# Performance work log

Measured on AMD Instinct MI355X. Metric: run time of the kernel, lower is better.

## Reference

```python
import jax, jax.numpy as jnp
import numpy as np

N_NODES = 100000
N_EDGES = 1600000
N_GRAPHS = 256
IN_C = 64
HID = 128
OUT = 128
BN_EPS = 1e-5


def setup_inputs() -> dict:
    key = jax.random.key(0)
    ks = jax.random.split(key, 24)
    x = jax.random.normal(ks[0], (N_NODES, IN_C), jnp.float32)
    edge_index = jax.random.randint(ks[1], (2, N_EDGES), 0, N_NODES, dtype=jnp.int64 if jax.config.jax_enable_x64 else jnp.int32)
    batch = jnp.sort(jax.random.randint(ks[2], (N_NODES,), 0, N_GRAPHS))

    def lin(k, i, o):
        return (jax.random.normal(k, (i, o), jnp.float32) / np.float32(np.sqrt(i)))

    d = {"x": x, "edge_index": edge_index, "batch": batch}
    in_dims = [IN_C, HID, HID]
    for l in range(3):
        d[f"w1_{l}"] = lin(ks[3 + 6 * l], in_dims[l], HID)
        d[f"b1_{l}"] = jnp.zeros((HID,), jnp.float32)
        d[f"w2_{l}"] = lin(ks[4 + 6 * l], HID, HID)
        d[f"b2_{l}"] = jnp.zeros((HID,), jnp.float32)
        d[f"gamma_{l}"] = jnp.ones((HID,), jnp.float32)
        d[f"beta_{l}"] = jnp.zeros((HID,), jnp.float32)
    d["proj_w"] = lin(ks[22], HID, OUT)
    d["proj_b"] = jnp.zeros((OUT,), jnp.float32)
    return d


def _gin_forward(x, edge_index, batch, layers, proj_w, proj_b):
    src, dst = edge_index[0], edge_index[1]
    h = x
    for (w1, b1, w2, b2, g, b) in layers:
        # GINConv (eps=0, aggr='add'): MLP(h_i + sum_{j->i} h_j)
        agg = jax.ops.segment_sum(h[src], dst, num_segments=h.shape[0])
        z = h + agg
        z = jax.nn.relu(z @ w1 + b1) @ w2 + b2
        # BatchNorm1d, training mode (biased batch stats)
        mean = z.mean(axis=0)
        var = z.var(axis=0)
        z = (z - mean) * jax.lax.rsqrt(var + BN_EPS) * g + b
        h = jax.nn.relu(z)
    # global_mean_pool over graph ids
    s = jax.ops.segment_sum(h, batch, num_segments=N_GRAPHS)
    cnt = jax.ops.segment_sum(jnp.ones((h.shape[0], 1), h.dtype), batch, num_segments=N_GRAPHS)
    hg = s / jnp.maximum(cnt, 1.0)
    return hg @ proj_w + proj_b


def reference(x, edge_index, batch,
              w1_0, b1_0, w2_0, b2_0, gamma_0, beta_0,
              w1_1, b1_1, w2_1, b2_1, gamma_1, beta_1,
              w1_2, b1_2, w2_2, b2_2, gamma_2, beta_2,
              proj_w, proj_b):
    layers = [
        (w1_0, b1_0, w2_0, b2_0, gamma_0, beta_0),
        (w1_1, b1_1, w2_1, b2_1, gamma_1, beta_1),
        (w1_2, b1_2, w2_2, b2_2, gamma_2, beta_2),
    ]
    return _gin_forward(x, edge_index, batch, layers, proj_w, proj_b)
```

## Files before the change

kernel.cpp:

```cpp
#include <hip/hip_runtime.h>

#define N_NODES 100000
#define N_EDGES 1600000
#define N_GRAPHS 256
#define HID 128
#define BN_EPS 1e-5f

#define NT 1563
#define EB 4096
#define RB 391
#define PB 1563

typedef __bf16 bf16x8 __attribute__((ext_vector_type(8)));
typedef __bf16 bf16x4 __attribute__((ext_vector_type(4)));
typedef __bf16 bf16x2 __attribute__((ext_vector_type(2)));
typedef float f32x4 __attribute__((ext_vector_type(4)));

__global__ __launch_bounds__(256) void setup_kernel(
    const float* __restrict__ x, __bf16* __restrict__ xb,
    const float* __restrict__ wa, const float* __restrict__ wb,
    const float* __restrict__ wc, const float* __restrict__ wd,
    const float* __restrict__ we, const float* __restrict__ wf,
    __bf16* __restrict__ wt,
    const int* __restrict__ batch, int* __restrict__ counts,
    const int* __restrict__ ei, int* __restrict__ tcnt) {
  __shared__ int hist[NT];
  int b = blockIdx.x;
  if (b < 6250) {
    int idx = b * 256 + threadIdx.x;
    if (idx >= N_NODES * 16) return;
    f32x4 v = ((const f32x4*)x)[idx];
    bf16x4 o = {(__bf16)v[0], (__bf16)v[1], (__bf16)v[2], (__bf16)v[3]};
    ((bf16x4*)xb)[idx] = o;
  } else if (b < 6250 + 352) {
    int idx = (b - 6250) * 256 + threadIdx.x;
    if (idx >= 90112) return;
    const float* w;
    int K, local;
    if (idx < 8192) { w = wa; K = 64; local = idx; }
    else {
      int s = (idx - 8192) / 16384;
      local = (idx - 8192) - s * 16384;
      K = 128;
      w = (s == 0) ? wb : (s == 1) ? wc : (s == 2) ? wd : (s == 3) ? we : wf;
    }
    int n = local / K, k = local - n * K;
    wt[idx] = (__bf16)w[k * 128 + n];
  } else if (b < 6609) {
    int t = (b - 6602) * 256 + threadIdx.x;
    int r0 = t * 64;
    if (r0 >= N_NODES) return;
    int rend = min(r0 + 64, N_NODES);
    int curg = batch[r0], cnt = 0;
    for (int r = r0; r < rend; r++) {
      int g = batch[r];
      if (g != curg) {
        atomicAdd(&counts[curg], cnt);
        curg = g;
        cnt = 1;
      } else {
        cnt++;
      }
    }
    atomicAdd(&counts[curg], cnt);
  } else {
    int t = threadIdx.x;
    for (int i = t; i < NT; i += 256) hist[i] = 0;
    __syncthreads();
    int base = (b - 6609) * EB;
#pragma unroll 4
    for (int i = 0; i < EB / 256; i++) {
      int e = base + i * 256 + t;
      if (e < N_EDGES) atomicAdd(&hist[ei[N_EDGES + e] >> 6], 1);
    }
    __syncthreads();
    for (int i = t; i < NT; i += 256) {
      int h = hist[i];
      if (h) atomicAdd(&tcnt[i], h);
    }
  }
}

__global__ __launch_bounds__(256) void tile_scan_kernel(const int* __restrict__ tcnt,
                                                        int* __restrict__ tstart,
                                                        int* __restrict__ gcursor) {
  __shared__ int ps[256];
  int t = threadIdx.x;
  const int CH = (NT + 255) / 256;
  int lo = t * CH, hi = min(lo + CH, NT);
  int s = 0;
  for (int i = lo; i < hi; i++) s += tcnt[i];
  ps[t] = s;
  __syncthreads();
  for (int off = 1; off < 256; off <<= 1) {
    int v = ps[t];
    int u = (t >= off) ? ps[t - off] : 0;
    __syncthreads();
    ps[t] = v + u;
    __syncthreads();
  }
  int base = (t == 0) ? 0 : ps[t - 1];
  for (int i = lo; i < hi; i++) {
    tstart[i] = base;
    gcursor[i] = base;
    base += tcnt[i];
  }
  if (t == 0) tstart[NT] = N_EDGES;
}

__global__ __launch_bounds__(256) void reorder2_kernel(const int* __restrict__ ei,
                                                       int* __restrict__ gcursor,
                                                       int* __restrict__ epack) {
  __shared__ int hist[NT];
  int t = threadIdx.x;
  for (int i = t; i < NT; i += 256) hist[i] = 0;
  __syncthreads();
  int base = blockIdx.x * EB;
#pragma unroll 4
  for (int i = 0; i < EB / 256; i++) {
    int e = base + i * 256 + t;
    if (e < N_EDGES) atomicAdd(&hist[ei[N_EDGES + e] >> 6], 1);
  }
  __syncthreads();
  for (int i = t; i < NT; i += 256) {
    int h = hist[i];
    if (h) hist[i] = atomicAdd(&gcursor[i], h);
  }
  __syncthreads();
#pragma unroll 4
  for (int i = 0; i < EB / 256; i++) {
    int e = base + i * 256 + t;
    if (e < N_EDGES) {
      int d = ei[N_EDGES + e];
      int s = ei[e];
      int pos = atomicAdd(&hist[d >> 6], 1);
      epack[pos] = (s << 6) | (d & 63);
    }
  }
}

__global__ __launch_bounds__(256) void row_sort_kernel(const int* __restrict__ tstart,
                                                       const int* __restrict__ epack,
                                                       int* __restrict__ starts,
                                                       int* __restrict__ srcs) {
  __shared__ int cnt[64];
  __shared__ int rbase[65];
  __shared__ int rofs[64];
  int t = threadIdx.x, b = blockIdx.x;
  int ts = tstart[b], te = tstart[b + 1];
  if (t < 64) cnt[t] = 0;
  __syncthreads();
  for (int i = ts + t; i < te; i += 256) atomicAdd(&cnt[epack[i] & 63], 1);
  __syncthreads();
  if (t == 0) {
    int a = 0;
    for (int r = 0; r < 64; r++) { rbase[r] = a; a += cnt[r]; }
    rbase[64] = a;
  }
  __syncthreads();
  if (t < 64) rofs[t] = ts + rbase[t];
  if (t <= 64) {
    int gr = b * 64 + t;
    if (gr <= N_NODES) starts[gr] = ts + rbase[t];
  }
  __syncthreads();
  for (int i = ts + t; i < te; i += 256) {
    int p = epack[i];
    int pos = atomicAdd(&rofs[p & 63], 1);
    srcs[pos] = p >> 6;
  }
}

template <int C, bool BN>
__global__ __launch_bounds__(256) void gather_kernel(const __bf16* __restrict__ h,
                                                     const float* __restrict__ accum,
                                                     const float* __restrict__ gamma,
                                                     const float* __restrict__ beta,
                                                     const int* __restrict__ starts,
                                                     const int* __restrict__ srcs,
                                                     __bf16* __restrict__ z) {
  const int lane = threadIdx.x & 63;
  const int row = __builtin_amdgcn_readfirstlane(blockIdx.x * 4 + (threadIdx.x >> 6));
  const int e0 = starts[row], e1 = starts[row + 1];

  if constexpr (C == 128) {
    float a0 = 0.f, a1 = 0.f, b0 = 0.f, b1 = 0.f;
    if constexpr (BN) {
      const int c0 = lane * 2, c1 = c0 + 1;
      const float invN = 1.f / (float)N_NODES;
      float m0 = accum[c0] * invN, m1 = accum[c1] * invN;
      float v0 = accum[HID + c0] * invN - m0 * m0;
      float v1 = accum[HID + c1] * invN - m1 * m1;
      a0 = gamma[c0] * rsqrtf(v0 + BN_EPS);
      a1 = gamma[c1] * rsqrtf(v1 + BN_EPS);
      b0 = beta[c0] - m0 * a0;
      b1 = beta[c1] - m1 * a1;
    }
#define ACCBN(vv, ss)                                                  \
    do {                                                               \
      if constexpr (BN) {                                              \
        ss.x += fmaxf(fmaf(a0, (float)(vv)[0], b0), 0.f);              \
        ss.y += fmaxf(fmaf(a1, (float)(vv)[1], b1), 0.f);              \
      } else {                                                         \
        ss.x += (float)(vv)[0];                                        \
        ss.y += (float)(vv)[1];                                        \
      }                                                                \
    } while (0)
    float2 s0 = {0.f, 0.f}, s1 = {0.f, 0.f}, s2 = {0.f, 0.f}, s3 = {0.f, 0.f};
    float2 s4 = {0.f, 0.f}, s5 = {0.f, 0.f}, s6 = {0.f, 0.f}, s7 = {0.f, 0.f};
    int e = e0;
    for (; e + 7 < e1; e += 8) {
      int i0 = srcs[e];
      int i1 = srcs[e + 1];
      int i2 = srcs[e + 2];
      int i3 = srcs[e + 3];
      int i4 = srcs[e + 4];
      int i5 = srcs[e + 5];
      int i6 = srcs[e + 6];
      int i7 = srcs[e + 7];
      bf16x2 v0 = *(const bf16x2*)(h + (size_t)i0 * 128 + lane * 2);
      bf16x2 v1 = *(const bf16x2*)(h + (size_t)i1 * 128 + lane * 2);
      bf16x2 v2 = *(const bf16x2*)(h + (size_t)i2 * 128 + lane * 2);
      bf16x2 v3 = *(const bf16x2*)(h + (size_t)i3 * 128 + lane * 2);
      bf16x2 v4 = *(const bf16x2*)(h + (size_t)i4 * 128 + lane * 2);
      bf16x2 v5 = *(const bf16x2*)(h + (size_t)i5 * 128 + lane * 2);
      bf16x2 v6 = *(const bf16x2*)(h + (size_t)i6 * 128 + lane * 2);
      bf16x2 v7 = *(const bf16x2*)(h + (size_t)i7 * 128 + lane * 2);
      ACCBN(v0, s0);
      ACCBN(v1, s1);
      ACCBN(v2, s2);
      ACCBN(v3, s3);
      ACCBN(v4, s4);
      ACCBN(v5, s5);
      ACCBN(v6, s6);
      ACCBN(v7, s7);
    }
    for (; e + 3 < e1; e += 4) {
      int i0 = srcs[e];
      int i1 = srcs[e + 1];
      int i2 = srcs[e + 2];
      int i3 = srcs[e + 3];
      bf16x2 v0 = *(const bf16x2*)(h + (size_t)i0 * 128 + lane * 2);
      bf16x2 v1 = *(const bf16x2*)(h + (size_t)i1 * 128 + lane * 2);
      bf16x2 v2 = *(const bf16x2*)(h + (size_t)i2 * 128 + lane * 2);
      bf16x2 v3 = *(const bf16x2*)(h + (size_t)i3 * 128 + lane * 2);
      ACCBN(v0, s0);
      ACCBN(v1, s1);
      ACCBN(v2, s2);
      ACCBN(v3, s3);
    }
    for (; e < e1; e++) {
      int i0 = srcs[e];
      bf16x2 vv = *(const bf16x2*)(h + (size_t)i0 * 128 + lane * 2);
      ACCBN(vv, s0);
    }
    bf16x2 sv = *(const bf16x2*)(h + (size_t)row * 128 + lane * 2);
    ACCBN(sv, s0);
    float tx = ((s0.x + s1.x) + (s2.x + s3.x)) + ((s4.x + s5.x) + (s6.x + s7.x));
    float ty = ((s0.y + s1.y) + (s2.y + s3.y)) + ((s4.y + s5.y) + (s6.y + s7.y));
    bf16x2 o = {(__bf16)tx, (__bf16)ty};
    *(bf16x2*)(z + (size_t)row * 128 + lane * 2) = o;
#undef ACCBN
  } else {
    float s0 = 0.f, s1 = 0.f, s2 = 0.f, s3 = 0.f;
    float s4 = 0.f, s5 = 0.f, s6 = 0.f, s7 = 0.f;
    int e = e0;
    for (; e + 7 < e1; e += 8) {
      int i0 = srcs[e];
      int i1 = srcs[e + 1];
      int i2 = srcs[e + 2];
      int i3 = srcs[e + 3];
      int i4 = srcs[e + 4];
      int i5 = srcs[e + 5];
      int i6 = srcs[e + 6];
      int i7 = srcs[e + 7];
      s0 += (float)h[(size_t)i0 * 64 + lane];
      s1 += (float)h[(size_t)i1 * 64 + lane];
      s2 += (float)h[(size_t)i2 * 64 + lane];
      s3 += (float)h[(size_t)i3 * 64 + lane];
      s4 += (float)h[(size_t)i4 * 64 + lane];
      s5 += (float)h[(size_t)i5 * 64 + lane];
      s6 += (float)h[(size_t)i6 * 64 + lane];
      s7 += (float)h[(size_t)i7 * 64 + lane];
    }
    for (; e + 3 < e1; e += 4) {
      int i0 = srcs[e];
      int i1 = srcs[e + 1];
      int i2 = srcs[e + 2];
      int i3 = srcs[e + 3];
      s0 += (float)h[(size_t)i0 * 64 + lane];
      s1 += (float)h[(size_t)i1 * 64 + lane];
      s2 += (float)h[(size_t)i2 * 64 + lane];
      s3 += (float)h[(size_t)i3 * 64 + lane];
    }
    for (; e < e1; e++) {
      int i0 = srcs[e];
      s0 += (float)h[(size_t)i0 * 64 + lane];
    }
    s0 += (float)h[(size_t)row * 64 + lane];
    float tot = ((s0 + s1) + (s2 + s3)) + ((s4 + s5) + (s6 + s7));
    z[(size_t)row * 64 + lane] = (__bf16)tot;
  }
}

template <int CIN>
__global__ __launch_bounds__(64, 2) void mlp_kernel(
    const __bf16* __restrict__ z, const __bf16* __restrict__ w1t,
    const float* __restrict__ b1, const __bf16* __restrict__ w2t,
    const float* __restrict__ b2, __bf16* __restrict__ u,
    float* __restrict__ part) {
  constexpr int TS = HID + 8;
  __shared__ __align__(16) __bf16 sm[64 * TS];

  const int lane = threadIdx.x;
  const int l16 = lane & 15;
  const int quad = lane >> 4;
  const int rowbase = blockIdx.x * 64;
  const int nvalid = min(64, N_NODES - rowbase);

  const f32x4 zero4 = {0.f, 0.f, 0.f, 0.f};
  f32x4 acc[8][4];

  {
#pragma unroll
    for (int ct = 0; ct < 8; ct++)
#pragma unroll
      for (int m = 0; m < 4; m++) acc[ct][m] = zero4;
#pragma unroll
    for (int ks = 0; ks < CIN / 32; ks++) {
      bf16x8 af[4];
#pragma unroll
      for (int m = 0; m < 4; m++) {
        int row = min(rowbase + m * 16 + l16, N_NODES - 1);
        af[m] = *(const bf16x8*)(z + (size_t)row * CIN + ks * 32 + quad * 8);
      }
#pragma unroll
      for (int ct = 0; ct < 8; ct++) {
        bf16x8 bfr = *(const bf16x8*)(w1t + (ct * 16 + l16) * CIN + ks * 32 + quad * 8);
#pragma unroll
        for (int m = 0; m < 4; m++)
          acc[ct][m] = __builtin_amdgcn_mfma_f32_16x16x32_bf16(af[m], bfr, acc[ct][m], 0, 0, 0);
      }
    }
#pragma unroll
    for (int ct = 0; ct < 8; ct++) {
      int col = ct * 16 + l16;
      float bias = b1[col];
#pragma unroll
      for (int m = 0; m < 4; m++)
#pragma unroll
        for (int r = 0; r < 4; r++) {
          float v = acc[ct][m][r] + bias;
          sm[(m * 16 + quad * 4 + r) * TS + col] = (__bf16)(v > 0.f ? v : 0.f);
        }
    }
  }

  {
#pragma unroll
    for (int ct = 0; ct < 8; ct++)
#pragma unroll
      for (int m = 0; m < 4; m++) acc[ct][m] = zero4;
#pragma unroll
    for (int ks = 0; ks < HID / 32; ks++) {
      bf16x8 af[4];
#pragma unroll
      for (int m = 0; m < 4; m++)
        af[m] = *(const bf16x8*)(sm + (m * 16 + l16) * TS + ks * 32 + quad * 8);
#pragma unroll
      for (int ct = 0; ct < 8; ct++) {
        bf16x8 bfr = *(const bf16x8*)(w2t + (ct * 16 + l16) * HID + ks * 32 + quad * 8);
#pragma unroll
        for (int m = 0; m < 4; m++)
          acc[ct][m] = __builtin_amdgcn_mfma_f32_16x16x32_bf16(af[m], bfr, acc[ct][m], 0, 0, 0);
      }
    }
  }

#pragma unroll
  for (int ct = 0; ct < 8; ct++) {
    int col = ct * 16 + l16;
    float bias = b2[col];
#pragma unroll
    for (int m = 0; m < 4; m++)
#pragma unroll
      for (int r = 0; r < 4; r++)
        sm[(m * 16 + quad * 4 + r) * TS + col] = (__bf16)(acc[ct][m][r] + bias);
  }

  for (int f = lane; f < nvalid * 16; f += 64) {
    int r = f >> 4, c8 = f & 15;
    bf16x8 v = *(const bf16x8*)(sm + r * TS + c8 * 8);
    *(bf16x8*)(u + (size_t)(rowbase + r) * HID + c8 * 8) = v;
  }

  {
    float s0 = 0.f, q0 = 0.f, s1 = 0.f, q1 = 0.f;
    for (int r = 0; r < nvalid; r++) {
      bf16x2 v = *(const bf16x2*)(sm + r * TS + lane * 2);
      float f0 = (float)v[0], f1 = (float)v[1];
      s0 += f0; q0 += f0 * f0;
      s1 += f1; q1 += f1 * f1;
    }
    float2 sp = {s0, s1}, qp = {q0, q1};
    *(float2*)(part + (size_t)blockIdx.x * 256 + lane * 2) = sp;
    *(float2*)(part + (size_t)blockIdx.x * 256 + HID + lane * 2) = qp;
  }
}

__global__ __launch_bounds__(256) void reduce_part_kernel(const float* __restrict__ part,
                                                          float* __restrict__ accum) {
  int t = threadIdx.x;
  float s = 0.f;
  for (int r = blockIdx.x; r < PB; r += gridDim.x)
    s += part[(size_t)r * 256 + t];
  atomicAdd(&accum[t], s);
}

__global__ __launch_bounds__(128) void bn_apply_pool_kernel(const __bf16* __restrict__ u,
                                                            const float* __restrict__ accum,
                                                            const float* __restrict__ gamma,
                                                            const float* __restrict__ beta,
                                                            const int* __restrict__ batch,
                                                            float* __restrict__ pool) {
  int c = threadIdx.x;
  int r0 = blockIdx.x * 64;
  if (r0 >= N_NODES) return;
  int rend = min(r0 + 64, N_NODES);
  const float invN = 1.f / (float)N_NODES;
  float mean = accum[c] * invN;
  float var = accum[HID + c] * invN - mean * mean;
  float a = gamma[c] * rsqrtf(var + BN_EPS);
  float b = beta[c] - mean * a;
  float accv = 0.f;
  int curg = -1;
  for (int r = r0; r < rend; r++) {
    int g = batch[r];
    if (g != curg) {
      if (curg >= 0) atomicAdd(&pool[curg * HID + c], accv);
      curg = g;
      accv = 0.f;
    }
    float v = (float)u[(size_t)r * HID + c];
    v = v * a + b;
    accv += (v > 0.f ? v : 0.f);
  }
  if (curg >= 0) atomicAdd(&pool[curg * HID + c], accv);
}

__global__ __launch_bounds__(128) void pool_proj_kernel(const float* __restrict__ pool,
                                                        const int* __restrict__ counts,
                                                        const float* __restrict__ pw,
                                                        const float* __restrict__ pb,
                                                        float* __restrict__ out) {
  int g = blockIdx.x;
  int c = threadIdx.x;
  __shared__ float hg[HID];
  float cnt = (float)max(counts[g], 1);
  hg[c] = pool[g * HID + c] / cnt;
  __syncthreads();
  float acc = pb[c];
#pragma unroll 8
  for (int k = 0; k < HID; k++) acc += hg[k] * pw[k * HID + c];
  out[g * HID + c] = acc;
}

extern "C" void kernel_launch(void* const* d_in, const int* in_sizes, int n_in,
                              void* d_out, int out_size, void* d_ws, size_t ws_size,
                              hipStream_t stream) {
  (void)in_sizes; (void)n_in; (void)out_size; (void)ws_size;
  const float* x = (const float*)d_in[0];
  const int* ei = (const int*)d_in[1];
  const int* batch = (const int*)d_in[2];
  const float* w1[3] = {(const float*)d_in[3], (const float*)d_in[9], (const float*)d_in[15]};
  const float* b1[3] = {(const float*)d_in[4], (const float*)d_in[10], (const float*)d_in[16]};
  const float* w2[3] = {(const float*)d_in[5], (const float*)d_in[11], (const float*)d_in[17]};
  const float* b2[3] = {(const float*)d_in[6], (const float*)d_in[12], (const float*)d_in[18]};
  const float* gm[3] = {(const float*)d_in[7], (const float*)d_in[13], (const float*)d_in[19]};
  const float* bt[3] = {(const float*)d_in[8], (const float*)d_in[14], (const float*)d_in[20]};
  const float* pw = (const float*)d_in[21];
  const float* pb = (const float*)d_in[22];
  float* out = (float*)d_out;

  char* ws = (char*)d_ws;
  __bf16* bufA = (__bf16*)ws;        ws += (size_t)N_NODES * HID * 2;
  __bf16* bufB = (__bf16*)ws;        ws += (size_t)N_NODES * HID * 2;
  __bf16* bufC = (__bf16*)ws;        ws += (size_t)N_NODES * HID * 2;
  __bf16* z0 = (__bf16*)ws;          ws += (size_t)N_NODES * 64 * 2;
  __bf16* xb = (__bf16*)ws;          ws += (size_t)N_NODES * 64 * 2;
  int* srcs = (int*)ws;              ws += (size_t)N_EDGES * 4;
  int* epack = (int*)ws;             ws += (size_t)N_EDGES * 4;
  int* starts = (int*)ws;            ws += (size_t)(N_NODES + 1) * 4;
  int* tcnt = (int*)ws;              ws += NT * 4;
  int* tstart = (int*)ws;            ws += (NT + 1) * 4;
  int* gcursor = (int*)ws;           ws += NT * 4;
  ws = (char*)(((uintptr_t)ws + 63) & ~(uintptr_t)63);
  float* part = (float*)ws;          ws += (size_t)PB * 256 * 4;
  __bf16* wt_all = (__bf16*)ws;      ws += 90112 * 2;
  ws = (char*)(((uintptr_t)ws + 63) & ~(uintptr_t)63);
  float* accum = (float*)ws;         ws += 3 * 256 * 4;
  float* pool = (float*)ws;          ws += N_GRAPHS * HID * 4;
  int* counts = (int*)ws;            ws += N_GRAPHS * 4;

  __bf16* w1t0 = wt_all;
  __bf16* w2t0 = wt_all + 8192;
  __bf16* w1t1 = wt_all + 24576;
  __bf16* w2t1 = wt_all + 40960;
  __bf16* w1t2 = wt_all + 57344;
  __bf16* w2t2 = wt_all + 73728;

  float* acc0 = accum;
  float* acc1 = accum + 256;
  float* acc2 = accum + 512;

  const int gat_blocks = (N_NODES + 3) / 4;

  hipMemsetAsync(accum, 0, 3 * 256 * 4 + (size_t)N_GRAPHS * HID * 4 + N_GRAPHS * 4, stream);
  hipMemsetAsync(tcnt, 0, NT * 4, stream);

  setup_kernel<<<7000, 256, 0, stream>>>(x, xb, w1[0], w2[0], w1[1], w2[1],
                                         w1[2], w2[2], wt_all, batch, counts, ei, tcnt);

  tile_scan_kernel<<<1, 256, 0, stream>>>(tcnt, tstart, gcursor);
  reorder2_kernel<<<RB, 256, 0, stream>>>(ei, gcursor, epack);
  row_sort_kernel<<<NT, 256, 0, stream>>>(tstart, epack, starts, srcs);

  gather_kernel<64, false><<<gat_blocks, 256, 0, stream>>>(xb, nullptr, nullptr, nullptr,
                                                           starts, srcs, z0);
  mlp_kernel<64><<<PB, 64, 0, stream>>>(z0, w1t0, b1[0], w2t0, b2[0], bufA, part);
  reduce_part_kernel<<<128, 256, 0, stream>>>(part, acc0);

  gather_kernel<128, true><<<gat_blocks, 256, 0, stream>>>(bufA, acc0, gm[0], bt[0],
                                                           starts, srcs, bufC);
  mlp_kernel<128><<<PB, 64, 0, stream>>>(bufC, w1t1, b1[1], w2t1, b2[1], bufB, part);
  reduce_part_kernel<<<128, 256, 0, stream>>>(part, acc1);

  gather_kernel<128, true><<<gat_blocks, 256, 0, stream>>>(bufB, acc1, gm[1], bt[1],
                                                           starts, srcs, bufC);
  mlp_kernel<128><<<PB, 64, 0, stream>>>(bufC, w1t2, b1[2], w2t2, b2[2], bufA, part);
  reduce_part_kernel<<<128, 256, 0, stream>>>(part, acc2);

  bn_apply_pool_kernel<<<NT, 128, 0, stream>>>(bufA, acc2, gm[2], bt[2], batch, pool);

  pool_proj_kernel<<<N_GRAPHS, 128, 0, stream>>>(pool, counts, pw, pb, out);
}
```

Baseline: 493.4 us.

## Stage MLP weights in LDS and run four waves per block

The MLP kernel now launches 256-thread blocks, each handling four 64-row tiles with one wave per tile. Both weight matrices are copied once per block into padded shared memory, so B-fragment loads read LDS instead of global memory. This is meant to cut repeated global and L2 weight traffic. In exchange, each block uses roughly 100 KB of LDS, which limits residency to one block per CU. The partial-stats buffer gains one padded slot, and waves past the last row write zeros to it.

After: 490.2 us, median of 2. Within noise of the previous version (-0.6%).

```diff
diff --git a/kernel.cpp b/kernel.cpp
--- a/kernel.cpp
+++ b/kernel.cpp
@@ -9,7 +9,8 @@
 #define NT 1563
 #define EB 4096
 #define RB 391
-#define PB 1563
+#define MBLK 391
+#define PB 1564
 
 typedef __bf16 bf16x8 __attribute__((ext_vector_type(8)));
 typedef __bf16 bf16x4 __attribute__((ext_vector_type(4)));
@@ -304,19 +305,44 @@
 }
 
 template <int CIN>
-__global__ __launch_bounds__(64, 2) void mlp_kernel(
+__global__ __launch_bounds__(256, 1) void mlp_kernel(
     const __bf16* __restrict__ z, const __bf16* __restrict__ w1t,
     const float* __restrict__ b1, const __bf16* __restrict__ w2t,
     const float* __restrict__ b2, __bf16* __restrict__ u,
     float* __restrict__ part) {
+  constexpr int CINP = CIN + 8;
   constexpr int TS = HID + 8;
-  __shared__ __align__(16) __bf16 sm[64 * TS];
-
-  const int lane = threadIdx.x;
+  __shared__ __align__(16) __bf16 w1s[128 * CINP];
+  __shared__ __align__(16) __bf16 w2s[128 * TS];
+  __shared__ __align__(16) __bf16 hsm[4 * 64 * TS];
+
+  const int tid = threadIdx.x;
+
+  for (int i = tid; i < 128 * (CIN / 8); i += 256) {
+    int r = i / (CIN / 8), c = i - r * (CIN / 8);
+    *(bf16x8*)(w1s + r * CINP + c * 8) = *(const bf16x8*)(w1t + r * CIN + c * 8);
+  }
+  for (int i = tid; i < 128 * 16; i += 256) {
+    int r = i >> 4, c = i & 15;
+    *(bf16x8*)(w2s + r * TS + c * 8) = *(const bf16x8*)(w2t + r * HID + c * 8);
+  }
+  __syncthreads();
+
+  const int wid = tid >> 6;
+  const int lane = tid & 63;
   const int l16 = lane & 15;
   const int quad = lane >> 4;
-  const int rowbase = blockIdx.x * 64;
+  const int wgid = blockIdx.x * 4 + wid;
+  const int rowbase = wgid * 64;
   const int nvalid = min(64, N_NODES - rowbase);
+  __bf16* sm = hsm + wid * 64 * TS;
+
+  if (nvalid <= 0) {
+    float2 z2 = {0.f, 0.f};
+    *(float2*)(part + (size_t)wgid * 256 + lane * 2) = z2;
+    *(float2*)(part + (size_t)wgid * 256 + HID + lane * 2) = z2;
+    return;
+  }
 
   const f32x4 zero4 = {0.f, 0.f, 0.f, 0.f};
   f32x4 acc[8][4];
@@ -336,7 +362,7 @@
       }
 #pragma unroll
       for (int ct = 0; ct < 8; ct++) {
-        bf16x8 bfr = *(const bf16x8*)(w1t + (ct * 16 + l16) * CIN + ks * 32 + quad * 8);
+        bf16x8 bfr = *(const bf16x8*)(w1s + (ct * 16 + l16) * CINP + ks * 32 + quad * 8);
 #pragma unroll
         for (int m = 0; m < 4; m++)
           acc[ct][m] = __builtin_amdgcn_mfma_f32_16x16x32_bf16(af[m], bfr, acc[ct][m], 0, 0, 0);
@@ -369,7 +395,7 @@
         af[m] = *(const bf16x8*)(sm + (m * 16 + l16) * TS + ks * 32 + quad * 8);
 #pragma unroll
       for (int ct = 0; ct < 8; ct++) {
-        bf16x8 bfr = *(const bf16x8*)(w2t + (ct * 16 + l16) * HID + ks * 32 + quad * 8);
+        bf16x8 bfr = *(const bf16x8*)(w2s + (ct * 16 + l16) * TS + ks * 32 + quad * 8);
 #pragma unroll
         for (int m = 0; m < 4; m++)
           acc[ct][m] = __builtin_amdgcn_mfma_f32_16x16x32_bf16(af[m], bfr, acc[ct][m], 0, 0, 0);
@@ -403,8 +429,8 @@
       s1 += f1; q1 += f1 * f1;
     }
     float2 sp = {s0, s1}, qp = {q0, q1};
-    *(float2*)(part + (size_t)blockIdx.x * 256 + lane * 2) = sp;
-    *(float2*)(part + (size_t)blockIdx.x * 256 + HID + lane * 2) = qp;
+    *(float2*)(part + (size_t)wgid * 256 + lane * 2) = sp;
+    *(float2*)(part + (size_t)wgid * 256 + HID + lane * 2) = qp;
   }
 }
 
@@ -527,17 +553,17 @@
 
   gather_kernel<64, false><<<gat_blocks, 256, 0, stream>>>(xb, nullptr, nullptr, nullptr,
                                                            starts, srcs, z0);
-  mlp_kernel<64><<<PB, 64, 0, stream>>>(z0, w1t0, b1[0], w2t0, b2[0], bufA, part);
+  mlp_kernel<64><<<MBLK, 256, 0, stream>>>(z0, w1t0, b1[0], w2t0, b2[0], bufA, part);
   reduce_part_kernel<<<128, 256, 0, stream>>>(part, acc0);
 
   gather_kernel<128, true><<<gat_blocks, 256, 0, stream>>>(bufA, acc0, gm[0], bt[0],
                                                            starts, srcs, bufC);
-  mlp_kernel<128><<<PB, 64, 0, stream>>>(bufC, w1t1, b1[1], w2t1, b2[1], bufB, part);
+  mlp_kernel<128><<<MBLK, 256, 0, stream>>>(bufC, w1t1, b1[1], w2t1, b2[1], bufB, part);
   reduce_part_kernel<<<128, 256, 0, stream>>>(part, acc1);
 
   gather_kernel<128, true><<<gat_blocks, 256, 0, stream>>>(bufB, acc1, gm[1], bt[1],
                                                            starts, srcs, bufC);
-  mlp_kernel<128><<<PB, 64, 0, stream>>>(bufC, w1t2, b1[2], w2t2, b2[2], bufA, part);
+  mlp_kernel<128><<<MBLK, 256, 0, stream>>>(bufC, w1t2, b1[2], w2t2, b2[2], bufA, part);
   reduce_part_kernel<<<128, 256, 0, stream>>>(part, acc2);
 
   bn_apply_pool_kernel<<<NT, 128, 0, stream>>>(bufA, acc2, gm[2], bt[2], batch, pool);
```
